# Optimization experiments

Measured on AMD Instinct MI355X. Metric: run time of the kernel, lower is better.

Reference implementation:

```python
import jax, jax.numpy as jnp
import numpy as np

# Loihi neuron constants (from a typical slayerSNN network.yaml)
I_DECAY = 1024.0   # current decay (of 4096)
V_DECAY = 128.0    # voltage decay (of 4096)
THETA = 100.0      # firing threshold


def spike_loihi(x):
    """Loihi CUBA neuron dynamics over trailing time axis. x: [..., T] weighted input."""
    xT = jnp.moveaxis(x, -1, 0)  # [T, ...]
    a_i = (4096.0 - I_DECAY) / 4096.0
    a_v = (4096.0 - V_DECAY) / 4096.0

    def step(carry, xt):
        u, v = carry
        u = a_i * u + xt           # synaptic current
        v = a_v * v + u            # membrane voltage
        s = (v >= THETA).astype(x.dtype)
        v = v * (1.0 - s)          # reset on spike
        return (u, v), s

    z = jnp.zeros(xT.shape[1:], x.dtype)
    _, s = jax.lax.scan(step, (z, z), xT)
    return jnp.moveaxis(s, 0, -1)


def delay_shift(x):
    """Shift spikes by 1 timestep along last axis (slayer.delayShift(spike, 1))."""
    return jnp.concatenate([jnp.zeros_like(x[..., :1]), x[..., :-1]], axis=-1)


def conv_t(x, w):
    """Per-timestep 2D conv, padding 1. x: [N,C,H,W,T], w: [O,I,3,3]."""
    N, C, H, W, T = x.shape
    xt = jnp.transpose(x, (0, 4, 1, 2, 3)).reshape(N * T, C, H, W)
    y = jax.lax.conv_general_dilated(xt, w, (1, 1), [(1, 1), (1, 1)],
                                     dimension_numbers=('NCHW', 'OIHW', 'NCHW'))
    O = w.shape[0]
    return jnp.transpose(y.reshape(N, T, O, H, W), (0, 2, 3, 4, 1))


def sum_pool2(x, w):
    """slayer.pool(2): 2x2 sum-pool scaled by (loaded) scalar pool weight."""
    N, C, H, W, T = x.shape
    return x.reshape(N, C, H // 2, 2, W // 2, 2, T).sum(axis=(3, 5)) * w


def setup_inputs() -> dict:
    key = jax.random.key(0)
    ks = jax.random.split(key, 8)
    N, T = 16, 128
    spike = jax.random.bernoulli(ks[0], 0.1, (N, 2, 40, 40, T)).astype(jnp.float32)
    conv1_w = jax.random.normal(ks[1], (8, 2, 3, 3), jnp.float32) * 0.5
    conv2_w = jax.random.normal(ks[2], (16, 8, 3, 3), jnp.float32) * 0.05
    conv3_w = jax.random.normal(ks[3], (32, 16, 3, 3), jnp.float32) * 0.05
    fc1_w = jax.random.normal(ks[4], (512, 10 * 10 * 32), jnp.float32) * 0.02
    pool1_w = jnp.asarray(1.1, jnp.float32)
    pool2_w = jnp.asarray(1.1, jnp.float32)
    return {"spike": spike, "conv1_w": conv1_w, "conv2_w": conv2_w,
            "conv3_w": conv3_w, "pool1_w": pool1_w, "pool2_w": pool2_w,
            "fc1_w": fc1_w}


def reference(spike, conv1_w, conv2_w, conv3_w, pool1_w, pool2_w, fc1_w):
    x = spike_loihi(conv_t(spike, conv1_w * 20.0))    # weightScale=20
    x = delay_shift(x)
    x = spike_loihi(sum_pool2(x, pool1_w))
    x = delay_shift(x)
    x = spike_loihi(conv_t(x, conv2_w * 100.0))       # weightScale=100
    x = delay_shift(x)
    x = spike_loihi(sum_pool2(x, pool2_w))
    x = delay_shift(x)
    x = spike_loihi(conv_t(x, conv3_w * 100.0))       # weightScale=100
    N, T = x.shape[0], x.shape[-1]
    x = x.reshape(N, -1, 1, 1, T)                     # [N, 3200, 1, 1, T]
    x = delay_shift(x)
    x = spike_loihi(jnp.einsum('nchwt,oc->nohwt', x, fc1_w))
    x = delay_shift(x)
    return x
```

## Files before the change

kernel.cpp:

```cpp
#include <hip/hip_runtime.h>
#include <stdint.h>


#define T 128
#define AI 0.75f
#define AV 0.96875f
#define THETA 100.0f

typedef __attribute__((ext_vector_type(8))) short v8s;
typedef __attribute__((ext_vector_type(16))) float v16f;

__device__ __forceinline__ void neuron_step(float x, float& u, float& v, float& s) {
    u = AI * u + x;
    v = AV * v + u;
    s = (v >= THETA) ? 1.0f : 0.0f;
    v = v * (1.0f - s);
}

__global__ __launch_bounds__(256) void conv1_scan(
    const float* __restrict__ in, const float* __restrict__ cw,
    uint8_t* __restrict__ sout)
{
    __shared__ float ldsF[64 * 130];
    int bid0 = blockIdx.x;
    int bid = (bid0 & 7) * 400 + (bid0 >> 3);
    int wg = bid % 5;
    int hy = (bid / 5) % 40;
    int n  = bid / 200;
    int tid = threadIdx.x;
    int wxl = tid >> 5, tt = tid & 31, t0 = tt * 4;
    int wx = wg * 8 + wxl;

    float4 tap[18];
    #pragma unroll
    for (int c = 0; c < 2; c++)
      #pragma unroll
      for (int dh = 0; dh < 3; dh++)
        #pragma unroll
        for (int dw = 0; dw < 3; dw++) {
            int q = c * 9 + dh * 3 + dw;
            int hh = hy + dh - 1, ww = wx + dw - 1;
            bool ok = (hh >= 0) && (hh < 40) && (ww >= 0) && (ww < 40);
            tap[q] = ok ? *(const float4*)(in +
                (((size_t)(n * 2 + c) * 40 + hh) * 40 + ww) * T + t0)
                        : make_float4(0.f, 0.f, 0.f, 0.f);
        }

    #pragma unroll
    for (int o = 0; o < 8; o++) {
        const float* wp = cw + o * 18;
        float a0 = 0.f, a1 = 0.f, a2 = 0.f, a3 = 0.f;
        #pragma unroll
        for (int q = 0; q < 18; q++) {
            a0 += wp[q] * tap[q].x;  a1 += wp[q] * tap[q].y;
            a2 += wp[q] * tap[q].z;  a3 += wp[q] * tap[q].w;
        }
        float* xr = &ldsF[(o * 8 + wxl) * 130 + t0];
        xr[0] = a0 * 20.0f; xr[1] = a1 * 20.0f;
        xr[2] = a2 * 20.0f; xr[3] = a3 * 20.0f;
    }
    __syncthreads();
    if (tid < 64) {
        int o = tid >> 3, wxl2 = tid & 7;
        float u = 0.f, v = 0.f;
        uint32_t ob[32];
        const float* xr = &ldsF[tid * 130];
        #pragma unroll
        for (int tb = 0; tb < 32; tb++) {
            float s0, s1, s2, s3;
            neuron_step(xr[tb * 4 + 0], u, v, s0);
            neuron_step(xr[tb * 4 + 1], u, v, s1);
            neuron_step(xr[tb * 4 + 2], u, v, s2);
            neuron_step(xr[tb * 4 + 3], u, v, s3);
            ob[tb] = (uint32_t)s0 | ((uint32_t)s1 << 8) |
                     ((uint32_t)s2 << 16) | ((uint32_t)s3 << 24);
        }
        uint32_t* op = (uint32_t*)(sout +
            (((size_t)(n * 8 + o) * 40 + hy) * 40 + wg * 8 + wxl2) * T);
        #pragma unroll
        for (int k = 0; k < 8; k++)
            *(uint4*)&op[k * 4] =
                make_uint4(ob[k*4], ob[k*4+1], ob[k*4+2], ob[k*4+3]);
    }
}

template<int C, int HO, int WO>
__global__ __launch_bounds__(320) void pool_pad(
    const uint8_t* __restrict__ in, const float* __restrict__ pw_ptr,
    uint16_t* __restrict__ sP)
{
    constexpr int CB = 320 / C;
    constexpr int GP = (HO * WO) / CB;
    __shared__ uint8_t raw[320 * 132];
    uint32_t* ldsF = (uint32_t*)raw;
    uint8_t*  sbuf = raw;

    int bid = blockIdx.x;
    int grp = bid % GP, n = bid / GP;
    int tid = threadIdx.x;
    float pw = pw_ptr[0];

    float u = 0.f, v = 0.f;
    uint32_t ob[32];
    uint32_t carry = 0;

    #pragma unroll
    for (int tb = 0; tb < 2; tb++) {
        __syncthreads();
        #pragma unroll
        for (int k = 0; k < 4; k++) {
            int f = tid + k * 320;
            int row = f >> 2, q = f & 3;
            int c = row / CB, p = row % CB;
            int hw = grp * CB + p;
            int wx = hw % WO, hy = hw / WO;
            const uint8_t* p00 = in +
                (((size_t)(n * C + c) * (2 * HO) + 2 * hy) * (2 * WO) + 2 * wx) * T;
            int off = tb * 64 + q * 16;
            uint4 a = *(const uint4*)(p00 + off);
            uint4 b = *(const uint4*)(p00 + T + off);
            uint4 cc = *(const uint4*)(p00 + 2 * WO * T + off);
            uint4 d = *(const uint4*)(p00 + 2 * WO * T + T + off);
            *(uint4*)&ldsF[row * 20 + q * 4] =
                make_uint4(a.x + b.x + cc.x + d.x, a.y + b.y + cc.y + d.y,
                           a.z + b.z + cc.z + d.z, a.w + b.w + cc.w + d.w);
        }
        __syncthreads();
        #pragma unroll
        for (int q = 0; q < 4; q++) {
            uint4 w = *(const uint4*)&ldsF[tid * 20 + q * 4];
            uint32_t words[4] = {w.x, w.y, w.z, w.w};
            #pragma unroll
            for (int j = 0; j < 4; j++) {
                uint32_t cur = words[j];
                uint32_t del = (cur << 8) | carry;
                carry = cur >> 24;
                float s0, s1, s2, s3;
                neuron_step(pw * (float)(del & 0xffu),         u, v, s0);
                neuron_step(pw * (float)((del >> 8) & 0xffu),  u, v, s1);
                neuron_step(pw * (float)((del >> 16) & 0xffu), u, v, s2);
                neuron_step(pw * (float)((del >> 24) & 0xffu), u, v, s3);
                ob[tb * 16 + q * 4 + j] = (uint32_t)s0 | ((uint32_t)s1 << 8) |
                                          ((uint32_t)s2 << 16) | ((uint32_t)s3 << 24);
            }
        }
    }

    __syncthreads();
    #pragma unroll
    for (int j = 0; j < 32; j++)
        *(uint32_t*)&sbuf[tid * 132 + j * 4] = ob[j];
    __syncthreads();

    constexpr int CHK = CB * 128;
    #pragma unroll
    for (int k = 0; k < CHK / 320; k++) {
        int ci = k * 320 + tid;
        int p = ci >> 7, tau = ci & 127;
        int hw = grp * CB + p;
        int wx = hw % WO, hy = hw / WO;
        uint32_t wb[8];
        #pragma unroll
        for (int e = 0; e < 16; e += 2) {
            uint32_t lo = 0u, hi = 0u;
            if (tau >= 1) {
                if (e < C)     lo = sbuf[(e * CB + p) * 132 + tau - 1] ? 0x3F80u : 0u;
                if (e + 1 < C) hi = sbuf[((e + 1) * CB + p) * 132 + tau - 1] ? 0x3F80u : 0u;
            }
            wb[e >> 1] = lo | (hi << 16);
        }
        uint16_t* dst = sP + ((size_t)((n * (HO + 2) + hy + 1) * (WO + 2)
                                       + wx + 1)) * 2048 + tau * 16;
        *(uint4*)dst       = make_uint4(wb[0], wb[1], wb[2], wb[3]);
        *(uint4*)(dst + 8) = make_uint4(wb[4], wb[5], wb[6], wb[7]);
    }
}

__global__ __launch_bounds__(256) void prep(
    const float* __restrict__ fw, const float* __restrict__ c2w,
    const float* __restrict__ c3w, uint16_t* __restrict__ bs,
    uint16_t* __restrict__ apk, uint16_t* __restrict__ s2P,
    uint16_t* __restrict__ s4P)
{
    int bid = blockIdx.x;
    int tid = threadIdx.x;
    if (bid < 1600) {
        int i = bid * 256 + tid;
        float4 wv = *(const float4*)(fw + i * 4);
        float w4[4] = {wv.x, wv.y, wv.z, wv.w};
        uint16_t h[4], m[4], l[4];
        #pragma unroll
        for (int j = 0; j < 4; j++) {
            uint32_t b0 = __float_as_uint(w4[j]);
            h[j] = (uint16_t)(b0 >> 16);
            float r1 = w4[j] - __uint_as_float(b0 & 0xFFFF0000u);
            uint32_t b1 = __float_as_uint(r1);
            m[j] = (uint16_t)(b1 >> 16);
            float r2 = r1 - __uint_as_float(b1 & 0xFFFF0000u);
            l[j] = (uint16_t)(__float_as_uint(r2) >> 16);
        }
        *(ushort4*)(bs +       0 + i * 4) = make_ushort4(h[0], h[1], h[2], h[3]);
        *(ushort4*)(bs + 1638400 + i * 4) = make_ushort4(m[0], m[1], m[2], m[3]);
        *(ushort4*)(bs + 3276800 + i * 4) = make_ushort4(l[0], l[1], l[2], l[3]);
    } else if (bid < 1614) {
        int unit = (bid - 1600) * 4 + (tid >> 6);
        if (unit >= 54) return;
        int conv = unit / 27;
        int plane = (unit % 27) / 9;
        int dlt = unit % 9;
        int lane = tid & 63;
        int o = lane & 31, chi = (lane >> 5) * 8;
        int CO = conv ? 32 : 16;
        int CI = conv ? 16 : 8;
        const float* Wp = conv ? c3w : c2w;
        uint32_t wb[4] = {0u, 0u, 0u, 0u};
        #pragma unroll
        for (int e = 0; e < 8; e++) {
            int c = chi + e;
            float w = (o < CO && c < CI) ? Wp[((size_t)o * CI + c) * 9 + dlt] : 0.f;
            uint32_t b0 = __float_as_uint(w);
            uint16_t hi = (uint16_t)(b0 >> 16);
            float r1 = w - __uint_as_float(b0 & 0xFFFF0000u);
            uint32_t b1 = __float_as_uint(r1);
            uint16_t md = (uint16_t)(b1 >> 16);
            float r2 = r1 - __uint_as_float(b1 & 0xFFFF0000u);
            uint16_t lo = (uint16_t)(__float_as_uint(r2) >> 16);
            uint32_t pv = (plane == 0) ? hi : ((plane == 1) ? md : lo);
            wb[e >> 1] |= pv << ((e & 1) * 16);
        }
        *(uint4*)(apk + ((size_t)conv * 27 + plane * 9 + dlt) * 512 + lane * 8) =
            make_uint4(wb[0], wb[1], wb[2], wb[3]);
    } else {
        int hid = bid - 1614;
        uint8_t* dst;
        if (hid < 1344) {
            int n = hid / 84, r = hid % 84;
            int hy, wx;
            if (r < 22)      { hy = 0;  wx = r; }
            else if (r < 44) { hy = 21; wx = r - 22; }
            else { int r2 = r - 44; hy = 1 + (r2 >> 1); wx = (r2 & 1) ? 21 : 0; }
            dst = (uint8_t*)s2P + ((size_t)(n * 484) + hy * 22 + wx) * 4096;
        } else {
            int h2 = hid - 1344;
            int n = h2 / 44, r = h2 % 44;
            int hy, wx;
            if (r < 12)      { hy = 0;  wx = r; }
            else if (r < 24) { hy = 11; wx = r - 12; }
            else { int r2 = r - 24; hy = 1 + (r2 >> 1); wx = (r2 & 1) ? 11 : 0; }
            dst = (uint8_t*)s4P + ((size_t)(n * 144) + hy * 12 + wx) * 4096;
        }
        *(uint4*)(dst + tid * 16) = make_uint4(0u, 0u, 0u, 0u);
    }
}

template<int COUT, int PB, int H, int W>
__global__ __launch_bounds__(256, 2) void conv_scan_mfma(
    const uint16_t* __restrict__ sP, const uint16_t* __restrict__ apk,
    float scale, uint8_t* __restrict__ sout)
{
    constexpr int ROWS = COUT * PB;
    __shared__ float ldsF[ROWS * 130];
    constexpr int HW = H * W;
    constexpr int GP = HW / PB;
    int per = (16 * GP) >> 3;
    int vbid = (blockIdx.x & 7) * per + (blockIdx.x >> 3);
    int n = vbid / GP, grp = vbid % GP;
    int tid = threadIdx.x;
    int wv = tid >> 6, lane = tid & 63;
    int l31 = lane & 31, lhi = lane >> 5;
    int t0 = wv * 32;

    const uint16_t* ap = apk + (size_t)lane * 8;
    v8s a0[9], a1[9], a2[9];
    #pragma unroll
    for (int d = 0; d < 9; d++) {
        a0[d] = *(const v8s*)(ap + d * 512);
        a1[d] = *(const v8s*)(ap + (9 + d) * 512);
        a2[d] = *(const v8s*)(ap + (18 + d) * 512);
    }

    #pragma unroll
    for (int p = 0; p < PB; p++) {
        int hw = grp * PB + p;
        int hy = hw / W, wx = hw % W;
        v8s bfr[9];
        #pragma unroll
        for (int d = 0; d < 9; d++) {
            int dh = d / 3, dw = d % 3;
            const uint16_t* src = sP
                + ((size_t)((n * (H + 2) + hy + dh) * (W + 2) + wx + dw)) * 2048
                + (t0 + l31) * 16 + lhi * 8;
            bfr[d] = *(const v8s*)src;
        }
        v16f ac0, ac1, ac2;
        #pragma unroll
        for (int e = 0; e < 16; e++) { ac0[e] = 0.f; ac1[e] = 0.f; ac2[e] = 0.f; }
        #pragma unroll
        for (int d = 0; d < 9; d++) {
            ac0 = __builtin_amdgcn_mfma_f32_32x32x16_bf16(a0[d], bfr[d], ac0, 0, 0, 0);
            ac1 = __builtin_amdgcn_mfma_f32_32x32x16_bf16(a1[d], bfr[d], ac1, 0, 0, 0);
            ac2 = __builtin_amdgcn_mfma_f32_32x32x16_bf16(a2[d], bfr[d], ac2, 0, 0, 0);
        }
        constexpr int NR = (COUT == 32) ? 16 : 8;
        #pragma unroll
        for (int r = 0; r < NR; r++) {
            int o = (r & 3) + 8 * (r >> 2) + 4 * lhi;
            ldsF[(o * PB + p) * 130 + t0 + l31] =
                (ac0[r] + ac1[r] + ac2[r]) * scale;
        }
    }
    __syncthreads();
    if (tid < ROWS) {
        int o = tid / PB, p = tid % PB;
        int hw = grp * PB + p;
        float u = 0.f, v = 0.f;
        uint32_t ob[32];
        const float* xr = &ldsF[tid * 130];
        #pragma unroll
        for (int tb = 0; tb < 32; tb++) {
            float2 xa = *(const float2*)(xr + tb * 4);
            float2 xb = *(const float2*)(xr + tb * 4 + 2);
            float s0, s1, s2, s3;
            neuron_step(xa.x, u, v, s0); neuron_step(xa.y, u, v, s1);
            neuron_step(xb.x, u, v, s2); neuron_step(xb.y, u, v, s3);
            ob[tb] = (uint32_t)s0 | ((uint32_t)s1 << 8) |
                     ((uint32_t)s2 << 16) | ((uint32_t)s3 << 24);
        }
        uint32_t* op = (uint32_t*)(sout + ((size_t)(n * COUT + o) * HW + hw) * 128);
        #pragma unroll
        for (int k = 0; k < 8; k++)
            *(uint4*)&op[k * 4] =
                make_uint4(ob[k*4], ob[k*4+1], ob[k*4+2], ob[k*4+3]);
    }
}

__global__ __launch_bounds__(256) void sT_bf16(
    const uint8_t* __restrict__ s5, uint16_t* __restrict__ At)
{
    __shared__ uint8_t tile[64 * 132];
    int bid = blockIdx.x;
    int n = bid / 50;
    int c0 = (bid % 50) * 64;
    int tid = threadIdx.x;
    {
        int row = tid >> 2, q = tid & 3;
        const uint8_t* src = s5 + ((size_t)(n * 3200 + c0 + row)) * T + q * 32;
        *(uint4*)&tile[row * 132 + q * 32]      = *(const uint4*)src;
        *(uint4*)&tile[row * 132 + q * 32 + 16] = *(const uint4*)(src + 16);
    }
    __syncthreads();
    int t = tid >> 1, half = tid & 1;
    uint32_t wb[16];
    if (t == 0) {
        #pragma unroll
        for (int j = 0; j < 16; j++) wb[j] = 0u;
    } else {
        #pragma unroll
        for (int j = 0; j < 16; j++) {
            uint32_t lo = tile[(half * 32 + 2 * j) * 132 + (t - 1)] ? 0x3F80u : 0u;
            uint32_t hi = tile[(half * 32 + 2 * j + 1) * 132 + (t - 1)] ? 0x3F80u : 0u;
            wb[j] = lo | (hi << 16);
        }
    }
    uint16_t* dst = At + ((size_t)(n * 128 + t)) * 3200 + c0 + half * 32;
    #pragma unroll
    for (int k = 0; k < 4; k++)
        *(uint4*)(dst + k * 8) = make_uint4(wb[k*4], wb[k*4+1], wb[k*4+2], wb[k*4+3]);
}

#define GLDS16(g, s) __builtin_amdgcn_global_load_lds( \
    (const __attribute__((address_space(1))) uint32_t*)(g), \
    (__attribute__((address_space(3))) uint32_t*)(s), 16, 0, 0)

__global__ __launch_bounds__(512, 4) void fc_gemm_mfma(
    const uint16_t* __restrict__ At,
    const uint16_t* __restrict__ Bs,
    float* __restrict__ ypart)
{
    __shared__ uint8_t lds[65536];
    int bid0 = blockIdx.x;
    int bid = (bid0 & 7) * 80 + (bid0 >> 3);
    int n  = bid & 15;
    int ob = (bid >> 4) & 3;
    int ks = bid >> 6;
    int o0 = ob * 128;
    int cbase = ks * 320;

    int tid = threadIdx.x;
    int w8 = tid >> 6;
    int wm = w8 >> 2;
    int wn = w8 & 3;
    int lane = tid & 63;
    int l31 = lane & 31;
    int lhi = lane >> 5;
    int rb = lane >> 3;
    int gsw = (lane & 7) ^ (rb & 7);

    v16f acc[2];
    #pragma unroll
    for (int mi = 0; mi < 2; mi++)
        #pragma unroll
        for (int e = 0; e < 16; e++) acc[mi][e] = 0.0f;

    const uint16_t* Abase = At + (size_t)(n * 128) * 3200 + gsw * 8;

    for (int kc = 0; kc < 5; kc++) {
        int c0 = cbase + kc * 64;
        #pragma unroll
        for (int i = 0; i < 2; i++) {
            int cid = i * 8 + w8;
            const uint16_t* src = Abase + (size_t)(cid * 8 + rb) * 3200 + c0;
            GLDS16(src, lds + cid * 1024);
        }
        #pragma unroll
        for (int j = 0; j < 6; j++) {
            int cid = j * 8 + w8;
            int f0 = cid * 1024;
            int s = f0 >> 14;
            int r = ((f0 & 16383) >> 7) + rb;
            const uint16_t* src = Bs + (size_t)(s * 512 + o0 + r) * 3200
                                     + c0 + gsw * 8;
            GLDS16(src, lds + 16384 + f0);
        }
        __syncthreads();
        #pragma unroll
        for (int kf = 0; kf < 4; kf++) {
            int gc = kf * 2 + lhi;
            v8s av[2];
            #pragma unroll
            for (int mi = 0; mi < 2; mi++) {
                int t = wm * 64 + mi * 32 + l31;
                av[mi] = *(const v8s*)(lds + t * 128 + ((gc ^ (t & 7)) << 4));
            }
            #pragma unroll
            for (int s = 0; s < 3; s++) {
                int r = wn * 32 + l31;
                v8s bv = *(const v8s*)(lds + 16384 + s * 16384 + r * 128
                                       + ((gc ^ (r & 7)) << 4));
                #pragma unroll
                for (int mi = 0; mi < 2; mi++)
                    acc[mi] = __builtin_amdgcn_mfma_f32_32x32x16_bf16(
                        av[mi], bv, acc[mi], 0, 0, 0);
            }
        }
        __syncthreads();
    }
    float* yp = ypart + (size_t)ks * 1048576 + (size_t)n * 65536;
    int o = o0 + wn * 32 + l31;
    #pragma unroll
    for (int mi = 0; mi < 2; mi++) {
        #pragma unroll
        for (int r = 0; r < 16; r++) {
            int trow = wm * 64 + mi * 32 + (r & 3) + 8 * (r >> 2) + 4 * lhi;
            yp[trow * 512 + o] = acc[mi][r];
        }
    }
}

__global__ __launch_bounds__(256) void fc_reduce(
    const float4* __restrict__ yp, float4* __restrict__ ys)
{
    int id = blockIdx.x * 256 + threadIdx.x;
    float4 x = yp[id];
    #pragma unroll
    for (int k = 1; k < 10; k++) {
        float4 y = yp[(size_t)k * 262144 + id];
        x.x += y.x; x.y += y.y; x.z += y.z; x.w += y.w;
    }
    ys[id] = x;
}

__global__ __launch_bounds__(64) void fc_scan(
    const float* __restrict__ ysum,
    float* __restrict__ out)
{
    int id = blockIdx.x * 64 + threadIdx.x;
    int o = id & 511;
    int n = id >> 9;
    float u = 0.f, v = 0.f;
    float prev = 0.f;
    for (int tb = 0; tb < T / 4; tb++) {
        float b0, b1, b2, b3;
        float x, s;
        x = ysum[(n * T + tb * 4 + 0) * 512 + o]; neuron_step(x, u, v, s); b0 = prev; prev = s;
        x = ysum[(n * T + tb * 4 + 1) * 512 + o]; neuron_step(x, u, v, s); b1 = prev; prev = s;
        x = ysum[(n * T + tb * 4 + 2) * 512 + o]; neuron_step(x, u, v, s); b2 = prev; prev = s;
        x = ysum[(n * T + tb * 4 + 3) * 512 + o]; neuron_step(x, u, v, s); b3 = prev; prev = s;
        *(float4*)&out[((size_t)(n * 512 + o)) * T + tb * 4] = make_float4(b0, b1, b2, b3);
    }
}

extern "C" void kernel_launch(void* const* d_in, const int* in_sizes, int n_in,
                              void* d_out, int out_size, void* d_ws, size_t ws_size,
                              hipStream_t stream) {
    const float* spike = (const float*)d_in[0];
    const float* c1w   = (const float*)d_in[1];
    const float* c2w   = (const float*)d_in[2];
    const float* c3w   = (const float*)d_in[3];
    const float* p1w   = (const float*)d_in[4];
    const float* p2w   = (const float*)d_in[5];
    const float* fcw   = (const float*)d_in[6];
    float* out = (float*)d_out;

    char* ws = (char*)d_ws;
    uint8_t*  s1    = (uint8_t*)(ws);
    uint16_t* Bs16  = (uint16_t*)(ws + 26214400);
    uint16_t* Apk   = (uint16_t*)(ws + 36044800);
    uint16_t* s2P   = (uint16_t*)(ws + 36100096);
    uint8_t*  s3    = (uint8_t*)(ws + 67819520);
    uint16_t* s4P   = (uint16_t*)(ws + 80926720);
    uint8_t*  s5    = (uint8_t*)(ws + 90363904);
    uint16_t* At16  = (uint16_t*)(ws + 96917504);
    float*    ypart = (float*)(ws + 110024704);
    float*    ysumb = (float*)(ws + 151967744);

    prep<<<3662, 256, 0, stream>>>(fcw, c2w, c3w, Bs16, Apk, s2P, s4P);
    conv1_scan<<<3200, 256, 0, stream>>>(spike, c1w, s1);

    pool_pad<8, 20, 20><<<160, 320, 0, stream>>>(s1, p1w, s2P);
    conv_scan_mfma<16, 4, 20, 20><<<1600, 256, 0, stream>>>(s2P, Apk, 100.0f, s3);

    pool_pad<16, 10, 10><<<80, 320, 0, stream>>>(s3, p2w, s4P);
    conv_scan_mfma<32, 2, 10, 10><<<800, 256, 0, stream>>>(s4P, Apk + 13824, 100.0f, s5);

    sT_bf16<<<800, 256, 0, stream>>>(s5, At16);
    fc_gemm_mfma<<<640, 512, 0, stream>>>(At16, Bs16, ypart);
    fc_reduce<<<1024, 256, 0, stream>>>((const float4*)ypart, (float4*)ysumb);
    fc_scan<<<128, 64, 0, stream>>>(ysumb, out);
}
```

Before: 244.0 us.

## Restructure conv1_scan so all threads run the neuron scan over time chunks

Each conv1_scan block now covers a whole 40-wide row instead of an 8-wide slice. It processes the time axis in four 32-step chunks, and after each chunk all 320 threads run the recurrent neuron scan for one (channel, column) pair. Before, only 64 of 256 threads did the serial scan over 128 steps while the rest sat idle. The change spreads the scan across every thread and carries u/v state between chunks, at the cost of extra barriers per chunk and fewer, larger blocks (640 instead of 3200).

```diff
diff --git a/kernel.cpp b/kernel.cpp
--- a/kernel.cpp
+++ b/kernel.cpp
@@ -17,56 +17,62 @@
     v = v * (1.0f - s);
 }
 
-__global__ __launch_bounds__(256) void conv1_scan(
+__global__ __launch_bounds__(320, 3) void conv1_scan(
     const float* __restrict__ in, const float* __restrict__ cw,
     uint8_t* __restrict__ sout)
 {
-    __shared__ float ldsF[64 * 130];
+    __shared__ float ldsX[320 * 35];
     int bid0 = blockIdx.x;
-    int bid = (bid0 & 7) * 400 + (bid0 >> 3);
-    int wg = bid % 5;
-    int hy = (bid / 5) % 40;
-    int n  = bid / 200;
+    int bid = (bid0 & 7) * 80 + (bid0 >> 3);
+    int hy = bid % 40;
+    int n  = bid / 40;
     int tid = threadIdx.x;
-    int wxl = tid >> 5, tt = tid & 31, t0 = tt * 4;
-    int wx = wg * 8 + wxl;
-
-    float4 tap[18];
-    #pragma unroll
-    for (int c = 0; c < 2; c++)
-      #pragma unroll
-      for (int dh = 0; dh < 3; dh++)
-        #pragma unroll
-        for (int dw = 0; dw < 3; dw++) {
-            int q = c * 9 + dh * 3 + dw;
-            int hh = hy + dh - 1, ww = wx + dw - 1;
-            bool ok = (hh >= 0) && (hh < 40) && (ww >= 0) && (ww < 40);
-            tap[q] = ok ? *(const float4*)(in +
-                (((size_t)(n * 2 + c) * 40 + hh) * 40 + ww) * T + t0)
-                        : make_float4(0.f, 0.f, 0.f, 0.f);
-        }
-
-    #pragma unroll
-    for (int o = 0; o < 8; o++) {
-        const float* wp = cw + o * 18;
-        float a0 = 0.f, a1 = 0.f, a2 = 0.f, a3 = 0.f;
-        #pragma unroll
-        for (int q = 0; q < 18; q++) {
-            a0 += wp[q] * tap[q].x;  a1 += wp[q] * tap[q].y;
-            a2 += wp[q] * tap[q].z;  a3 += wp[q] * tap[q].w;
-        }
-        float* xr = &ldsF[(o * 8 + wxl) * 130 + t0];
-        xr[0] = a0 * 20.0f; xr[1] = a1 * 20.0f;
-        xr[2] = a2 * 20.0f; xr[3] = a3 * 20.0f;
-    }
-    __syncthreads();
-    if (tid < 64) {
-        int o = tid >> 3, wxl2 = tid & 7;
-        float u = 0.f, v = 0.f;
-        uint32_t ob[32];
-        const float* xr = &ldsF[tid * 130];
-        #pragma unroll
-        for (int tb = 0; tb < 32; tb++) {
+    int wx = tid >> 3, tt = tid & 7;
+    int so = tid / 40, swx = tid % 40;
+
+    bool okh[3] = {hy > 0, true, hy < 39};
+    bool okw[3] = {wx > 0, true, wx < 39};
+
+    float u = 0.f, v = 0.f;
+    uint32_t* op = (uint32_t*)(sout +
+        (((size_t)(n * 8 + so) * 40 + hy) * 40 + swx) * T);
+
+    #pragma unroll 1
+    for (int ch = 0; ch < 4; ch++) {
+        int t0 = ch * 32 + tt * 4;
+        float4 tap[18];
+        #pragma unroll
+        for (int c = 0; c < 2; c++)
+          #pragma unroll
+          for (int dh = 0; dh < 3; dh++)
+            #pragma unroll
+            for (int dw = 0; dw < 3; dw++) {
+                int q = c * 9 + dh * 3 + dw;
+                int gy = hy + dh - 1, gx = wx + dw - 1;
+                bool ok = okh[dh] && okw[dw];
+                tap[q] = ok ? *(const float4*)(in +
+                    (((size_t)(n * 2 + c) * 40 + gy) * 40 + gx) * T + t0)
+                            : make_float4(0.f, 0.f, 0.f, 0.f);
+            }
+        __syncthreads();
+        #pragma unroll
+        for (int o = 0; o < 8; o++) {
+            const float* wp = cw + o * 18;
+            float a0 = 0.f, a1 = 0.f, a2 = 0.f, a3 = 0.f;
+            #pragma unroll
+            for (int q = 0; q < 18; q++) {
+                a0 += wp[q] * tap[q].x;  a1 += wp[q] * tap[q].y;
+                a2 += wp[q] * tap[q].z;  a3 += wp[q] * tap[q].w;
+            }
+            float* xr = &ldsX[(o * 40 + wx) * 35 + tt * 4];
+            xr[0] = a0 * 20.0f; xr[1] = a1 * 20.0f;
+            xr[2] = a2 * 20.0f; xr[3] = a3 * 20.0f;
+        }
+        __syncthreads();
+        const float* xr = &ldsX[tid * 35];
+        uint32_t ob[8];
+        #pragma unroll
+        for (int tb = 0; tb < 8; tb++) {
             float s0, s1, s2, s3;
             neuron_step(xr[tb * 4 + 0], u, v, s0);
             neuron_step(xr[tb * 4 + 1], u, v, s1);
@@ -75,12 +81,8 @@
             ob[tb] = (uint32_t)s0 | ((uint32_t)s1 << 8) |
                      ((uint32_t)s2 << 16) | ((uint32_t)s3 << 24);
         }
-        uint32_t* op = (uint32_t*)(sout +
-            (((size_t)(n * 8 + o) * 40 + hy) * 40 + wg * 8 + wxl2) * T);
-        #pragma unroll
-        for (int k = 0; k < 8; k++)
-            *(uint4*)&op[k * 4] =
-                make_uint4(ob[k*4], ob[k*4+1], ob[k*4+2], ob[k*4+3]);
+        *(uint4*)&op[ch * 8]     = make_uint4(ob[0], ob[1], ob[2], ob[3]);
+        *(uint4*)&op[ch * 8 + 4] = make_uint4(ob[4], ob[5], ob[6], ob[7]);
     }
 }
 
@@ -515,7 +517,7 @@
     float*    ysumb = (float*)(ws + 151967744);
 
     prep<<<3662, 256, 0, stream>>>(fcw, c2w, c3w, Bs16, Apk, s2P, s4P);
-    conv1_scan<<<3200, 256, 0, stream>>>(spike, c1w, s1);
+    conv1_scan<<<640, 320, 0, stream>>>(spike, c1w, s1);
 
     pool_pad<8, 20, 20><<<160, 320, 0, stream>>>(s1, p1w, s2P);
     conv_scan_mfma<16, 4, 20, 20><<<1600, 256, 0, stream>>>(s2P, Apk, 100.0f, s3);
```

After: 303.8 us. +24.5%, slower.
